# Optimization experiments

Measured on AMD Instinct MI355X. Metric: run time of the kernel, lower is better.

The kernel has to match this reference:

```python
import jax, jax.numpy as jnp
import numpy as np

BATCH = 4194304

# Heaviside step (IF neuron single-step fire, v_reset=0) -- forward only.
def heav(x):
    return (x >= 0.0).astype(x.dtype)

# SNN logic gates (thresholds from the torch module)
def AND(a, b):
    return heav(a + b - 1.5)

def OR(a, b):
    return heav(a + b - 0.5)

def NOT(a):
    return heav((1.0 - a) - 0.5)

def MUX(s, a, b):
    # OR(AND(s,a), AND(NOT(s),b)) : s=1 -> a, s=0 -> b
    return OR(AND(s, a), AND(NOT(s), b))

def or_tree(xs):
    cur = list(xs)
    while len(cur) > 1:
        nxt = []
        for i in range(0, len(cur), 2):
            if i + 1 < len(cur):
                nxt.append(OR(cur[i], cur[i + 1]))
            else:
                nxt.append(cur[i])
        cur = nxt
    return cur[0]


def setup_inputs() -> dict:
    key = jax.random.key(0)
    P = (jax.random.uniform(key, (BATCH, 8)) < 0.5).astype(jnp.float32)
    return {"P": P}


def reference(P):
    p = [P[..., i:i + 1] for i in range(8)]  # little-endian bits, each [B,1]
    z = jnp.zeros_like(p[0])

    # --- PriorityEncoder8: leading-one detector (one-hot) ---
    inhibits = [None] * 8
    curr = p[7]
    inhibits[6] = curr
    for i in range(5, -1, -1):
        curr = OR(p[i + 1], curr)
        inhibits[i] = curr
    valid = []
    for i in range(8):
        if i == 7:
            valid.append(p[7])
        else:
            valid.append(AND(p[i], NOT(inhibits[i])))
    v = valid

    # --- ShiftAmountEncoder8to3: one-hot -> 3-bit binary ---
    s0 = or_tree([v[6], v[4], v[2], v[0]])
    s1 = or_tree([v[5], v[4], v[1], v[0]])
    s2 = or_tree([v[3], v[2], v[1], v[0]])
    shift_amt = jnp.concatenate([s0, s1, s2], axis=-1)  # [B,3]

    # --- ExponentAdjuster: one-hot -> 5-bit exponent adjustment ---
    any_valid = or_tree([v[i] for i in range(8)])
    is_zero = NOT(any_valid)
    e0 = or_tree([v[7], v[5], v[3], v[1], is_zero, z, z, z])
    e1 = or_tree([v[5], v[4], v[1], v[0], z, z, z, z])
    e2 = or_tree([v[5], v[4], v[3], v[2], z, z, z, z])
    e3 = or_tree([v[5], v[4], v[3], v[2], v[1], v[0], is_zero, z])
    e4 = or_tree([v[5], v[4], v[3], v[2], v[1], v[0], is_zero, z])
    exp_adj = jnp.concatenate([e0, e1, e2, e3, e4], axis=-1)  # [B,5]

    # --- top-level wiring ---
    sticky_extra = p[0]
    overflow = p[7]
    p_pre = p[1:] + [z]  # drop LSB, append zero (list of [B,1])

    # --- BarrelShifter8 (left shift by {s2,s1,s0} = {4,2,1}) ---
    stage1 = [MUX(s2, p_pre[i - 4] if i >= 4 else z, p_pre[i]) for i in range(8)]
    stage2 = [MUX(s1, stage1[i - 2] if i >= 2 else z, stage1[i]) for i in range(8)]
    stage3 = [MUX(s0, stage2[i - 1] if i >= 1 else z, stage2[i]) for i in range(8)]
    p_norm = jnp.concatenate(stage3, axis=-1)  # [B,8]

    return (p_norm, exp_adj, sticky_extra, overflow, shift_amt)
```

## Files before the change

### kernel.cpp

```cpp
#include <hip/hip_runtime.h>


__global__ __launch_bounds__(256) void snn_norm_kernel(
    const float* __restrict__ P, float* __restrict__ out, unsigned B)
{
    float* __restrict__ p_norm   = out;
    float* __restrict__ exp_adj  = out + (size_t)B * 8;
    float* __restrict__ sticky   = out + (size_t)B * 13;
    float* __restrict__ overflow = out + (size_t)B * 14;
    float* __restrict__ shamt    = out + (size_t)B * 15;

    const unsigned stride = gridDim.x * blockDim.x;
    for (unsigned r = blockIdx.x * blockDim.x + threadIdx.x; r < B; r += stride) {
        const float4 a = reinterpret_cast<const float4*>(P)[(size_t)r * 2];
        const float4 b = reinterpret_cast<const float4*>(P)[(size_t)r * 2 + 1];

        unsigned m = 0;
        m |= (a.x >= 0.5f) ? 1u   : 0u;
        m |= (a.y >= 0.5f) ? 2u   : 0u;
        m |= (a.z >= 0.5f) ? 4u   : 0u;
        m |= (a.w >= 0.5f) ? 8u   : 0u;
        m |= (b.x >= 0.5f) ? 16u  : 0u;
        m |= (b.y >= 0.5f) ? 32u  : 0u;
        m |= (b.z >= 0.5f) ? 64u  : 0u;
        m |= (b.w >= 0.5f) ? 128u : 0u;

        const int k = 31 - __clz((int)(m | 1u));
        const bool nz = (m != 0u);

        const unsigned shift = nz ? (7u - (unsigned)k) : 0u;
        const unsigned pn = ((m >> 1) << shift) & 0xFFu;

        const unsigned e0 = (unsigned)(k & 1) | (nz ? 0u : 1u);
        const unsigned e1 = (nz && ((k & 2) == 0)) ? 1u : 0u;
        const unsigned e2 = (nz && (k >= 2) && (k <= 5)) ? 1u : 0u;
        const unsigned e3 = (k <= 5) ? 1u : 0u;

        float4 o0, o1;
        o0.x = (float)( pn       & 1u);
        o0.y = (float)((pn >> 1) & 1u);
        o0.z = (float)((pn >> 2) & 1u);
        o0.w = (float)((pn >> 3) & 1u);
        o1.x = (float)((pn >> 4) & 1u);
        o1.y = (float)((pn >> 5) & 1u);
        o1.z = (float)((pn >> 6) & 1u);
        o1.w = (float)((pn >> 7) & 1u);
        reinterpret_cast<float4*>(p_norm)[(size_t)r * 2]     = o0;
        reinterpret_cast<float4*>(p_norm)[(size_t)r * 2 + 1] = o1;

        float* e = exp_adj + (size_t)r * 5;
        e[0] = (float)e0;
        e[1] = (float)e1;
        e[2] = (float)e2;
        e[3] = (float)e3;
        e[4] = (float)e3;

        sticky[r]   = (float)(m & 1u);
        overflow[r] = (float)(m >> 7);

        float* s = shamt + (size_t)r * 3;
        s[0] = (float)( shift       & 1u);
        s[1] = (float)((shift >> 1) & 1u);
        s[2] = (float)((shift >> 2) & 1u);
    }
}

extern "C" void kernel_launch(void* const* d_in, const int* in_sizes, int n_in,
                              void* d_out, int out_size, void* d_ws, size_t ws_size,
                              hipStream_t stream) {
    const float* P = (const float*)d_in[0];
    float* out = (float*)d_out;
    const unsigned B = (unsigned)(in_sizes[0] / 8);

    const int threads = 256;
    const int blocks = 2048;
    snn_norm_kernel<<<blocks, threads, 0, stream>>>(P, out, B);
}
```

Baseline: 390.6 us.

## Stage exp_adj and shift outputs through LDS for coalesced float4 stores

Each block now handles one 256-row tile. Per-row outputs go into shared memory first, then the block writes them back as contiguous float4 stores, replacing the stride-5 and stride-3 scalar global writes. The grid-stride loop is dropped in favour of one block per tile, which launches far more blocks. This costs one barrier and extra LDS traffic per tile, and the float4 reinterpretation of the stride-5 and stride-3 global output regions relies on alignment, which holds because TILE is a multiple of 4.

Result: no change. 385.2 us (-1.4%).

```diff
diff --git a/kernel.cpp b/kernel.cpp
--- a/kernel.cpp
+++ b/kernel.cpp
@@ -1,5 +1,7 @@
 #include <hip/hip_runtime.h>
 
+
+#define TILE 256
 
 __global__ __launch_bounds__(256) void snn_norm_kernel(
     const float* __restrict__ P, float* __restrict__ out, unsigned B)
@@ -10,10 +12,17 @@
     float* __restrict__ overflow = out + (size_t)B * 14;
     float* __restrict__ shamt    = out + (size_t)B * 15;
 
-    const unsigned stride = gridDim.x * blockDim.x;
-    for (unsigned r = blockIdx.x * blockDim.x + threadIdx.x; r < B; r += stride) {
-        const float4 a = reinterpret_cast<const float4*>(P)[(size_t)r * 2];
-        const float4 b = reinterpret_cast<const float4*>(P)[(size_t)r * 2 + 1];
+    __shared__ float lds_pn[TILE * 8];
+    __shared__ float lds_e [TILE * 5];
+    __shared__ float lds_sh[TILE * 3];
+
+    const unsigned tid = threadIdx.x;
+    const size_t tileRow = (size_t)blockIdx.x * TILE;
+    const size_t r = tileRow + tid;
+
+    if (r < B) {
+        const float4 a = reinterpret_cast<const float4*>(P)[r * 2];
+        const float4 b = reinterpret_cast<const float4*>(P)[r * 2 + 1];
 
         unsigned m = 0;
         m |= (a.x >= 0.5f) ? 1u   : 0u;
@@ -45,23 +54,49 @@
         o1.y = (float)((pn >> 5) & 1u);
         o1.z = (float)((pn >> 6) & 1u);
         o1.w = (float)((pn >> 7) & 1u);
-        reinterpret_cast<float4*>(p_norm)[(size_t)r * 2]     = o0;
-        reinterpret_cast<float4*>(p_norm)[(size_t)r * 2 + 1] = o1;
+        reinterpret_cast<float4*>(lds_pn)[tid * 2]     = o0;
+        reinterpret_cast<float4*>(lds_pn)[tid * 2 + 1] = o1;
 
-        float* e = exp_adj + (size_t)r * 5;
-        e[0] = (float)e0;
-        e[1] = (float)e1;
-        e[2] = (float)e2;
-        e[3] = (float)e3;
-        e[4] = (float)e3;
+        lds_e[tid * 5 + 0] = (float)e0;
+        lds_e[tid * 5 + 1] = (float)e1;
+        lds_e[tid * 5 + 2] = (float)e2;
+        lds_e[tid * 5 + 3] = (float)e3;
+        lds_e[tid * 5 + 4] = (float)e3;
+
+        lds_sh[tid * 3 + 0] = (float)( shift       & 1u);
+        lds_sh[tid * 3 + 1] = (float)((shift >> 1) & 1u);
+        lds_sh[tid * 3 + 2] = (float)((shift >> 2) & 1u);
 
         sticky[r]   = (float)(m & 1u);
         overflow[r] = (float)(m >> 7);
+    }
 
-        float* s = shamt + (size_t)r * 3;
-        s[0] = (float)( shift       & 1u);
-        s[1] = (float)((shift >> 1) & 1u);
-        s[2] = (float)((shift >> 2) & 1u);
+    __syncthreads();
+
+    if (tileRow + TILE <= B) {
+        float4* __restrict__ pnG = reinterpret_cast<float4*>(p_norm + tileRow * 8);
+        const float4* pnL = reinterpret_cast<const float4*>(lds_pn);
+        #pragma unroll
+        for (int i = 0; i < 2; ++i)
+            pnG[tid + i * 256] = pnL[tid + i * 256];
+
+        float4* __restrict__ eG = reinterpret_cast<float4*>(exp_adj + tileRow * 5);
+        const float4* eL = reinterpret_cast<const float4*>(lds_e);
+        for (int i = tid; i < TILE * 5 / 4; i += 256)
+            eG[i] = eL[i];
+
+        float4* __restrict__ sG = reinterpret_cast<float4*>(shamt + tileRow * 3);
+        const float4* sL = reinterpret_cast<const float4*>(lds_sh);
+        for (int i = tid; i < TILE * 3 / 4; i += 256)
+            sG[i] = sL[i];
+    } else {
+        const unsigned rows = (unsigned)(B - tileRow);
+        for (unsigned i = tid; i < rows * 8; i += 256)
+            p_norm[tileRow * 8 + i] = lds_pn[i];
+        for (unsigned i = tid; i < rows * 5; i += 256)
+            exp_adj[tileRow * 5 + i] = lds_e[i];
+        for (unsigned i = tid; i < rows * 3; i += 256)
+            shamt[tileRow * 3 + i] = lds_sh[i];
     }
 }
 
@@ -73,6 +108,6 @@
     const unsigned B = (unsigned)(in_sizes[0] / 8);
 
     const int threads = 256;
-    const int blocks = 2048;
+    const int blocks = (int)((B + TILE - 1) / TILE);
     snn_norm_kernel<<<blocks, threads, 0, stream>>>(P, out, B);
 }
```
